# Kernel optimization log

Measured on AMD Instinct MI355X. Metric: run time of the kernel, lower is better.

The kernel has to match this reference:

```python
import jax, jax.numpy as jnp
import numpy as np

B, IN, OUT = 1024, 512, 64000
EPS = 1e-12  # matches torch F.normalize eps


def setup_inputs() -> dict:
    key = jax.random.key(0)
    k1, k2, k3 = jax.random.split(key, 3)
    x = jax.random.normal(k1, (B, IN), dtype=jnp.float32)
    label = jax.random.randint(k2, (B,), 0, OUT)
    # xavier_uniform_ for weight [OUT, IN]: limit = sqrt(6 / (fan_in + fan_out))
    limit = float(np.sqrt(6.0 / (IN + OUT)))
    weight = jax.random.uniform(k3, (OUT, IN), dtype=jnp.float32, minval=-limit, maxval=limit)
    s = 50               # python scalar; set via _calculate_para but UNUSED in normfree output
    m = jnp.full((1,), 0.5, dtype=jnp.float32)  # margin
    return {"x": x, "label": label, "weight": weight, "s": s, "m": m}


def reference(x, label, weight, s, m):
    m = m.reshape(())
    cos_m, sin_m = jnp.cos(m), jnp.sin(m)
    # norm of raw input (the 'normfree' scale replacing s)
    norm = jnp.linalg.norm(x, axis=1, keepdims=True)            # [B, 1]
    xn = x / jnp.maximum(norm, EPS)                             # F.normalize(input)
    wn = weight / jnp.maximum(
        jnp.linalg.norm(weight, axis=1, keepdims=True), EPS)    # F.normalize(weight)
    cosine = xn @ wn.T                                          # [B, OUT]
    sine = jnp.sqrt(jnp.clip(1.0 - cosine * cosine, 0.0, None))
    phi = cosine * cos_m - sine * sin_m                         # cos(theta + m)
    # per-sample loop in torch == one-hot substitution only where cosine > 0
    onehot = jax.nn.one_hot(label, OUT, dtype=bool)             # [B, OUT]
    mod_cosine = jnp.where(onehot & (cosine > 0), phi, cosine)
    return norm * mod_cosine, wn
```

## Files before the change

kernel.cpp:

```cpp
#include <hip/hip_runtime.h>
#include <cstdint>

#define EPSN 1e-12f
static constexpr int B_ROWS = 1024;
static constexpr int IN_DIM = 512;
static constexpr int OUT_DIM = 64000;

typedef __attribute__((ext_vector_type(8))) short bf16x8;
typedef __attribute__((ext_vector_type(4))) float f32x4;

__device__ __forceinline__ unsigned short f2bf(float f) {
  uint32_t u = __builtin_bit_cast(uint32_t, f);
  u += 0x7fffu + ((u >> 16) & 1u);
  return (unsigned short)(u >> 16);
}

__device__ __forceinline__ float wave_sum(float v) {
#pragma unroll
  for (int off = 32; off; off >>= 1) v += __shfl_xor(v, off);
  return v;
}

__device__ __forceinline__ void async16(const void* g, void* l) {
  __builtin_amdgcn_global_load_lds((const __attribute__((address_space(1))) uint32_t*)g,
                                   (__attribute__((address_space(3))) uint32_t*)l, 16, 0, 0);
}

__global__ void wnorm_kernel(const float* __restrict__ Wg, float* __restrict__ wnOut,
                             unsigned short* __restrict__ wbf, int useBf) {
  int lane = threadIdx.x & 63;
  int row = blockIdx.x * 4 + (threadIdx.x >> 6);
  const float* src = Wg + (size_t)row * IN_DIM + lane * 8;
  float4 a = *(const float4*)src;
  float4 b = *(const float4*)(src + 4);
  float ss = a.x * a.x;
  ss = fmaf(a.y, a.y, ss); ss = fmaf(a.z, a.z, ss); ss = fmaf(a.w, a.w, ss);
  ss = fmaf(b.x, b.x, ss); ss = fmaf(b.y, b.y, ss); ss = fmaf(b.z, b.z, ss);
  ss = fmaf(b.w, b.w, ss);
  ss = wave_sum(ss);
  float inv = 1.0f / fmaxf(sqrtf(ss), EPSN);
  float4 wa, wb;
  wa.x = a.x * inv; wa.y = a.y * inv; wa.z = a.z * inv; wa.w = a.w * inv;
  wb.x = b.x * inv; wb.y = b.y * inv; wb.z = b.z * inv; wb.w = b.w * inv;
  float* dst = wnOut + (size_t)row * IN_DIM + lane * 8;
  *(float4*)dst = wa;
  *(float4*)(dst + 4) = wb;
  if (useBf) {
    uint4 u;
    u.x = (uint32_t)f2bf(wa.x) | ((uint32_t)f2bf(wa.y) << 16);
    u.y = (uint32_t)f2bf(wa.z) | ((uint32_t)f2bf(wa.w) << 16);
    u.z = (uint32_t)f2bf(wb.x) | ((uint32_t)f2bf(wb.y) << 16);
    u.w = (uint32_t)f2bf(wb.z) | ((uint32_t)f2bf(wb.w) << 16);
    *(uint4*)(wbf + (size_t)row * IN_DIM + lane * 8) = u;
  }
}

__global__ void prep_kernel(const float* __restrict__ X, const int* __restrict__ label,
                            const float* __restrict__ wn, float* __restrict__ norms,
                            float* __restrict__ fixdot, unsigned short* __restrict__ xbf) {
  int lane = threadIdx.x & 63;
  int row = blockIdx.x * 4 + (threadIdx.x >> 6);
  const float* src = X + (size_t)row * IN_DIM + lane * 8;
  float4 a = *(const float4*)src;
  float4 b = *(const float4*)(src + 4);
  uint4 u;
  u.x = (uint32_t)f2bf(a.x) | ((uint32_t)f2bf(a.y) << 16);
  u.y = (uint32_t)f2bf(a.z) | ((uint32_t)f2bf(a.w) << 16);
  u.z = (uint32_t)f2bf(b.x) | ((uint32_t)f2bf(b.y) << 16);
  u.w = (uint32_t)f2bf(b.z) | ((uint32_t)f2bf(b.w) << 16);
  *(uint4*)(xbf + (size_t)row * IN_DIM + lane * 8) = u;
  float ss = a.x * a.x;
  ss = fmaf(a.y, a.y, ss); ss = fmaf(a.z, a.z, ss); ss = fmaf(a.w, a.w, ss);
  ss = fmaf(b.x, b.x, ss); ss = fmaf(b.y, b.y, ss); ss = fmaf(b.z, b.z, ss);
  ss = fmaf(b.w, b.w, ss);
  ss = wave_sum(ss);
  int lab = label[row];
  const float* wsrc = wn + (size_t)lab * IN_DIM + lane * 8;
  float4 wa = *(const float4*)wsrc, wb = *(const float4*)(wsrc + 4);
  float d = a.x * wa.x;
  d = fmaf(a.y, wa.y, d); d = fmaf(a.z, wa.z, d); d = fmaf(a.w, wa.w, d);
  d = fmaf(b.x, wb.x, d); d = fmaf(b.y, wb.y, d); d = fmaf(b.z, wb.z, d);
  d = fmaf(b.w, wb.w, d);
  d = wave_sum(d);
  if (lane == 0) { norms[row] = sqrtf(ss); fixdot[row] = d; }
}

template <bool BF16B>
__global__ __launch_bounds__(512, 2) void gemm8_kernel(
    const unsigned short* __restrict__ Abf, const unsigned short* __restrict__ Bbf,
    const float* __restrict__ Bf32, const float* __restrict__ norms,
    const float* __restrict__ fixdot, const int* __restrict__ label,
    const float* __restrict__ mArr, float* __restrict__ out0) {
  __shared__ char smem[131072];

  const int t = threadIdx.x;
  int flat = blockIdx.x;
  int xcd = flat & 7;
  int wk = (flat >> 3) + xcd * 125;
  int mT = wk & 3, nT = wk >> 2;
  int rowA0 = mT * 256, rowB0 = nT * 256;

  int lane = t & 63;
  int wid = t >> 6;
  int wm = wid >> 2, wn2 = wid & 3;
  int rl = lane & 15, sl = lane >> 4;

  int r0 = t >> 2, q0 = (t & 3) ^ ((r0 >> 1) & 3);
  int r1 = (t + 512) >> 2, q1 = ((t + 512) & 3) ^ ((r1 >> 1) & 3);
  const unsigned short* aP0 = Abf + (size_t)(rowA0 + r0) * IN_DIM + q0 * 8;
  const unsigned short* aP1 = Abf + (size_t)(rowA0 + r1) * IN_DIM + q1 * 8;
  const unsigned short* bP0 = Bbf + (size_t)(rowB0 + r0) * IN_DIM + q0 * 8;
  const unsigned short* bP1 = Bbf + (size_t)(rowB0 + r1) * IN_DIM + q1 * 8;
  const float* bF0 = Bf32 + (size_t)(rowB0 + r0) * IN_DIM + q0 * 8;
  const float* bF1 = Bf32 + (size_t)(rowB0 + r1) * IN_DIM + q1 * 8;

  auto issueSub = [&](int sig) {
    int kt = sig >> 1, s = sig & 1, buf = kt & 1;
    char* aD = smem + buf * 65536 + s * 16384;
    char* bD = aD + 32768;
    int kcol = kt * 64 + s * 32;
    async16(aP0 + kcol, aD + t * 16);
    async16(aP1 + kcol, aD + (t + 512) * 16);
    if constexpr (BF16B) {
      async16(bP0 + kcol, bD + t * 16);
      async16(bP1 + kcol, bD + (t + 512) * 16);
    } else {
      float4 f0 = *(const float4*)(bF0 + kcol);
      float4 f1 = *(const float4*)(bF0 + kcol + 4);
      uint4 u;
      u.x = (uint32_t)f2bf(f0.x) | ((uint32_t)f2bf(f0.y) << 16);
      u.y = (uint32_t)f2bf(f0.z) | ((uint32_t)f2bf(f0.w) << 16);
      u.z = (uint32_t)f2bf(f1.x) | ((uint32_t)f2bf(f1.y) << 16);
      u.w = (uint32_t)f2bf(f1.z) | ((uint32_t)f2bf(f1.w) << 16);
      *(uint4*)(bD + t * 16) = u;
      f0 = *(const float4*)(bF1 + kcol);
      f1 = *(const float4*)(bF1 + kcol + 4);
      u.x = (uint32_t)f2bf(f0.x) | ((uint32_t)f2bf(f0.y) << 16);
      u.y = (uint32_t)f2bf(f0.z) | ((uint32_t)f2bf(f0.w) << 16);
      u.z = (uint32_t)f2bf(f1.x) | ((uint32_t)f2bf(f1.y) << 16);
      u.w = (uint32_t)f2bf(f1.z) | ((uint32_t)f2bf(f1.w) << 16);
      *(uint4*)(bD + (t + 512) * 16) = u;
    }
  };

  issueSub(0); issueSub(1); issueSub(2);

  f32x4 acc[8][4];
#pragma unroll
  for (int m = 0; m < 8; ++m)
#pragma unroll
    for (int n = 0; n < 4; ++n) acc[m][n] = (f32x4){0.f, 0.f, 0.f, 0.f};

#pragma unroll 1
  for (int sigma = 0; sigma < 16; ++sigma) {
    int kt = sigma >> 1, s = sigma & 1, buf = kt & 1;
    if constexpr (BF16B) {
      int remain = 15 - sigma;
      __builtin_amdgcn_sched_barrier(0);
      if (remain >= 2)      asm volatile("s_waitcnt vmcnt(8)" ::: "memory");
      else if (remain == 1) asm volatile("s_waitcnt vmcnt(4)" ::: "memory");
      else                  asm volatile("s_waitcnt vmcnt(0)" ::: "memory");
      __builtin_amdgcn_s_barrier();
      __builtin_amdgcn_sched_barrier(0);
    } else {
      __syncthreads();
    }
    const char* aB = smem + buf * 65536 + s * 16384;
    const char* bB = aB + 32768;
    bf16x8 av[8], bv[4];
#pragma unroll
    for (int m = 0; m < 8; ++m) {
      int r = wm * 128 + m * 16 + rl;
      av[m] = *(const bf16x8*)(aB + r * 64 + ((sl ^ ((r >> 1) & 3)) * 16));
    }
#pragma unroll
    for (int n = 0; n < 4; ++n) {
      int r = wn2 * 64 + n * 16 + rl;
      bv[n] = *(const bf16x8*)(bB + r * 64 + ((sl ^ ((r >> 1) & 3)) * 16));
    }
    if (sigma + 3 <= 15) issueSub(sigma + 3);
    __builtin_amdgcn_s_setprio(1);
#pragma unroll
    for (int n = 0; n < 4; ++n)
#pragma unroll
      for (int m = 0; m < 8; ++m)
        acc[m][n] = __builtin_amdgcn_mfma_f32_16x16x32_bf16(av[m], bv[n], acc[m][n], 0, 0, 0);
    __builtin_amdgcn_s_setprio(0);
    if constexpr (BF16B) {
      __builtin_amdgcn_s_barrier();
      __builtin_amdgcn_sched_barrier(0);
    } else {
      __syncthreads();
    }
  }

  float mm = mArr[0];
  float cm = cosf(mm), sm = sinf(mm);
  int rowb = rowA0 + wm * 128, colb = rowB0 + wn2 * 64;
#pragma unroll
  for (int m = 0; m < 8; ++m) {
#pragma unroll
    for (int q = 0; q < 4; ++q) {
      int R = rowb + m * 16 + sl * 4 + q;
      int lab = label[R];
      float nv = norms[R], fv = fixdot[R];
      float* orow = out0 + (size_t)R * OUT_DIM;
#pragma unroll
      for (int n = 0; n < 4; ++n) {
        int Cc = colb + n * 16 + rl;
        float val = acc[m][n][q];
        if (Cc == lab) {
          float c = fv / fmaxf(nv, EPSN);
          val = (c > 0.f) ? nv * (c * cm - sqrtf(fmaxf(1.f - c * c, 0.f)) * sm) : fv;
        }
        orow[Cc] = val;
      }
    }
  }
}

extern "C" void kernel_launch(void* const* d_in, const int* in_sizes, int n_in,
                              void* d_out, int out_size, void* d_ws, size_t ws_size,
                              hipStream_t stream) {
  const float* x = (const float*)d_in[0];
  const int* label = (const int*)d_in[1];
  const float* weight = (const float*)d_in[2];
  const float* mArr = (const float*)d_in[4];

  float* out0 = (float*)d_out;
  float* wnOut = out0 + (size_t)B_ROWS * OUT_DIM;

  char* ws = (char*)d_ws;
  float* norms = (float*)ws;
  float* fixdot = (float*)(ws + 4096);
  unsigned short* xbf = (unsigned short*)(ws + 8192);
  unsigned short* wbf = (unsigned short*)(ws + 8192 + 2ull * B_ROWS * IN_DIM);
  size_t need = 8192 + 2ull * B_ROWS * IN_DIM + 2ull * OUT_DIM * IN_DIM;
  bool useBf = ws_size >= need;

  wnorm_kernel<<<OUT_DIM / 4, 256, 0, stream>>>(weight, wnOut, wbf, useBf ? 1 : 0);
  prep_kernel<<<B_ROWS / 4, 256, 0, stream>>>(x, label, wnOut, norms, fixdot, xbf);
  if (useBf)
    gemm8_kernel<true><<<1000, 512, 0, stream>>>(xbf, wbf, wnOut, norms, fixdot,
                                                 label, mArr, out0);
  else
    gemm8_kernel<false><<<1000, 512, 0, stream>>>(xbf, wbf, wnOut, norms, fixdot,
                                                  label, mArr, out0);
}
```

Before: 199.0 us.

## Fuse weight normalization into GEMM, staging normalized bf16 B tiles in-kernel

Drops the separate weight-normalization kernel and the bf16 weight copy in workspace. Each GEMM block now computes inverse row norms for its 256 weight rows, writes one quarter of the normalized fp32 rows to the wn output, and converts fp32 weight to scaled bf16 while staging B into LDS with a 4-deep ring buffer. The prep kernel computes the label-row norm itself so it no longer depends on wn. This removes a full read-write pass over the 131MB weight plus the bf16 write and re-read. In exchange each weight tile is read in fp32 by all four M-tile blocks, with synchronous register-path B loads in the main loop and an extra norm pass at the start of every block.

Measured after the change: 284.5 us. +43.0%, slower.

```diff
diff --git a/kernel.cpp b/kernel.cpp
--- a/kernel.cpp
+++ b/kernel.cpp
@@ -26,37 +26,8 @@
                                    (__attribute__((address_space(3))) uint32_t*)l, 16, 0, 0);
 }
 
-__global__ void wnorm_kernel(const float* __restrict__ Wg, float* __restrict__ wnOut,
-                             unsigned short* __restrict__ wbf, int useBf) {
-  int lane = threadIdx.x & 63;
-  int row = blockIdx.x * 4 + (threadIdx.x >> 6);
-  const float* src = Wg + (size_t)row * IN_DIM + lane * 8;
-  float4 a = *(const float4*)src;
-  float4 b = *(const float4*)(src + 4);
-  float ss = a.x * a.x;
-  ss = fmaf(a.y, a.y, ss); ss = fmaf(a.z, a.z, ss); ss = fmaf(a.w, a.w, ss);
-  ss = fmaf(b.x, b.x, ss); ss = fmaf(b.y, b.y, ss); ss = fmaf(b.z, b.z, ss);
-  ss = fmaf(b.w, b.w, ss);
-  ss = wave_sum(ss);
-  float inv = 1.0f / fmaxf(sqrtf(ss), EPSN);
-  float4 wa, wb;
-  wa.x = a.x * inv; wa.y = a.y * inv; wa.z = a.z * inv; wa.w = a.w * inv;
-  wb.x = b.x * inv; wb.y = b.y * inv; wb.z = b.z * inv; wb.w = b.w * inv;
-  float* dst = wnOut + (size_t)row * IN_DIM + lane * 8;
-  *(float4*)dst = wa;
-  *(float4*)(dst + 4) = wb;
-  if (useBf) {
-    uint4 u;
-    u.x = (uint32_t)f2bf(wa.x) | ((uint32_t)f2bf(wa.y) << 16);
-    u.y = (uint32_t)f2bf(wa.z) | ((uint32_t)f2bf(wa.w) << 16);
-    u.z = (uint32_t)f2bf(wb.x) | ((uint32_t)f2bf(wb.y) << 16);
-    u.w = (uint32_t)f2bf(wb.z) | ((uint32_t)f2bf(wb.w) << 16);
-    *(uint4*)(wbf + (size_t)row * IN_DIM + lane * 8) = u;
-  }
-}
-
 __global__ void prep_kernel(const float* __restrict__ X, const int* __restrict__ label,
-                            const float* __restrict__ wn, float* __restrict__ norms,
+                            const float* __restrict__ Wg, float* __restrict__ norms,
                             float* __restrict__ fixdot, unsigned short* __restrict__ xbf) {
   int lane = threadIdx.x & 63;
   int row = blockIdx.x * 4 + (threadIdx.x >> 6);
@@ -69,29 +40,37 @@
   u.z = (uint32_t)f2bf(b.x) | ((uint32_t)f2bf(b.y) << 16);
   u.w = (uint32_t)f2bf(b.z) | ((uint32_t)f2bf(b.w) << 16);
   *(uint4*)(xbf + (size_t)row * IN_DIM + lane * 8) = u;
-  float ss = a.x * a.x;
-  ss = fmaf(a.y, a.y, ss); ss = fmaf(a.z, a.z, ss); ss = fmaf(a.w, a.w, ss);
-  ss = fmaf(b.x, b.x, ss); ss = fmaf(b.y, b.y, ss); ss = fmaf(b.z, b.z, ss);
-  ss = fmaf(b.w, b.w, ss);
-  ss = wave_sum(ss);
+  float ssx = a.x * a.x;
+  ssx = fmaf(a.y, a.y, ssx); ssx = fmaf(a.z, a.z, ssx); ssx = fmaf(a.w, a.w, ssx);
+  ssx = fmaf(b.x, b.x, ssx); ssx = fmaf(b.y, b.y, ssx); ssx = fmaf(b.z, b.z, ssx);
+  ssx = fmaf(b.w, b.w, ssx);
   int lab = label[row];
-  const float* wsrc = wn + (size_t)lab * IN_DIM + lane * 8;
+  const float* wsrc = Wg + (size_t)lab * IN_DIM + lane * 8;
   float4 wa = *(const float4*)wsrc, wb = *(const float4*)(wsrc + 4);
   float d = a.x * wa.x;
   d = fmaf(a.y, wa.y, d); d = fmaf(a.z, wa.z, d); d = fmaf(a.w, wa.w, d);
   d = fmaf(b.x, wb.x, d); d = fmaf(b.y, wb.y, d); d = fmaf(b.z, wb.z, d);
   d = fmaf(b.w, wb.w, d);
+  float ssw = wa.x * wa.x;
+  ssw = fmaf(wa.y, wa.y, ssw); ssw = fmaf(wa.z, wa.z, ssw); ssw = fmaf(wa.w, wa.w, ssw);
+  ssw = fmaf(wb.x, wb.x, ssw); ssw = fmaf(wb.y, wb.y, ssw); ssw = fmaf(wb.z, wb.z, ssw);
+  ssw = fmaf(wb.w, wb.w, ssw);
+  ssx = wave_sum(ssx);
   d = wave_sum(d);
-  if (lane == 0) { norms[row] = sqrtf(ss); fixdot[row] = d; }
-}
-
-template <bool BF16B>
-__global__ __launch_bounds__(512, 2) void gemm8_kernel(
-    const unsigned short* __restrict__ Abf, const unsigned short* __restrict__ Bbf,
-    const float* __restrict__ Bf32, const float* __restrict__ norms,
-    const float* __restrict__ fixdot, const int* __restrict__ label,
-    const float* __restrict__ mArr, float* __restrict__ out0) {
-  __shared__ char smem[131072];
+  ssw = wave_sum(ssw);
+  if (lane == 0) {
+    norms[row] = sqrtf(ssx);
+    fixdot[row] = d / fmaxf(sqrtf(ssw), EPSN);
+  }
+}
+
+__global__ __launch_bounds__(512, 2) void fused_kernel(
+    const float* __restrict__ Wg, const unsigned short* __restrict__ Abf,
+    const float* __restrict__ norms, const float* __restrict__ fixdot,
+    const int* __restrict__ label, const float* __restrict__ mArr,
+    float* __restrict__ out0, float* __restrict__ wnOut) {
+  __shared__ char smem[132096];
+  float* invnL = (float*)(smem + 131072);
 
   const int t = threadIdx.x;
   int flat = blockIdx.x;
@@ -105,45 +84,72 @@
   int wm = wid >> 2, wn2 = wid & 3;
   int rl = lane & 15, sl = lane >> 4;
 
-  int r0 = t >> 2, q0 = (t & 3) ^ ((r0 >> 1) & 3);
-  int r1 = (t + 512) >> 2, q1 = ((t + 512) & 3) ^ ((r1 >> 1) & 3);
-  const unsigned short* aP0 = Abf + (size_t)(rowA0 + r0) * IN_DIM + q0 * 8;
-  const unsigned short* aP1 = Abf + (size_t)(rowA0 + r1) * IN_DIM + q1 * 8;
-  const unsigned short* bP0 = Bbf + (size_t)(rowB0 + r0) * IN_DIM + q0 * 8;
-  const unsigned short* bP1 = Bbf + (size_t)(rowB0 + r1) * IN_DIM + q1 * 8;
-  const float* bF0 = Bf32 + (size_t)(rowB0 + r0) * IN_DIM + q0 * 8;
-  const float* bF1 = Bf32 + (size_t)(rowB0 + r1) * IN_DIM + q1 * 8;
-
-  auto issueSub = [&](int sig) {
-    int kt = sig >> 1, s = sig & 1, buf = kt & 1;
-    char* aD = smem + buf * 65536 + s * 16384;
-    char* bD = aD + 32768;
-    int kcol = kt * 64 + s * 32;
+#pragma unroll 1
+  for (int rr = 0; rr < 32; ++rr) {
+    int r = wid * 32 + rr;
+    const float* src = Wg + (size_t)(rowB0 + r) * IN_DIM + lane * 8;
+    float4 a = *(const float4*)src;
+    float4 b = *(const float4*)(src + 4);
+    float ss = a.x * a.x;
+    ss = fmaf(a.y, a.y, ss); ss = fmaf(a.z, a.z, ss); ss = fmaf(a.w, a.w, ss);
+    ss = fmaf(b.x, b.x, ss); ss = fmaf(b.y, b.y, ss); ss = fmaf(b.z, b.z, ss);
+    ss = fmaf(b.w, b.w, ss);
+    ss = wave_sum(ss);
+    float inv = 1.0f / fmaxf(sqrtf(ss), EPSN);
+    if (lane == 0) invnL[r] = inv;
+    if ((r >> 6) == mT) {
+      float* dst = wnOut + (size_t)(rowB0 + r) * IN_DIM + lane * 8;
+      float4 wa, wb;
+      wa.x = a.x * inv; wa.y = a.y * inv; wa.z = a.z * inv; wa.w = a.w * inv;
+      wb.x = b.x * inv; wb.y = b.y * inv; wb.z = b.z * inv; wb.w = b.w * inv;
+      *(float4*)dst = wa;
+      *(float4*)(dst + 4) = wb;
+    }
+  }
+  __syncthreads();
+
+  int r0 = t >> 2, q0 = t & 3;
+  int r1 = (t + 512) >> 2, q1 = (t + 512) & 3;
+  float inv0 = invnL[r0], inv1 = invnL[r1];
+  const float* bSrc0 = Wg + (size_t)(rowB0 + r0) * IN_DIM + q0 * 8;
+  const float* bSrc1 = Wg + (size_t)(rowB0 + r1) * IN_DIM + q1 * 8;
+  int bOff0 = r0 * 64 + ((q0 ^ ((r0 >> 1) & 3)) * 16);
+  int bOff1 = r1 * 64 + ((q1 ^ ((r1 >> 1) & 3)) * 16);
+
+  int ra0 = t >> 2, qa0 = (t & 3) ^ ((ra0 >> 1) & 3);
+  int ra1 = (t + 512) >> 2, qa1 = ((t + 512) & 3) ^ ((ra1 >> 1) & 3);
+  const unsigned short* aP0 = Abf + (size_t)(rowA0 + ra0) * IN_DIM + qa0 * 8;
+  const unsigned short* aP1 = Abf + (size_t)(rowA0 + ra1) * IN_DIM + qa1 * 8;
+
+  auto issueA = [&](int sig) {
+    char* aD = smem + (sig & 3) * 16384;
+    int kcol = sig * 32;
     async16(aP0 + kcol, aD + t * 16);
     async16(aP1 + kcol, aD + (t + 512) * 16);
-    if constexpr (BF16B) {
-      async16(bP0 + kcol, bD + t * 16);
-      async16(bP1 + kcol, bD + (t + 512) * 16);
-    } else {
-      float4 f0 = *(const float4*)(bF0 + kcol);
-      float4 f1 = *(const float4*)(bF0 + kcol + 4);
-      uint4 u;
-      u.x = (uint32_t)f2bf(f0.x) | ((uint32_t)f2bf(f0.y) << 16);
-      u.y = (uint32_t)f2bf(f0.z) | ((uint32_t)f2bf(f0.w) << 16);
-      u.z = (uint32_t)f2bf(f1.x) | ((uint32_t)f2bf(f1.y) << 16);
-      u.w = (uint32_t)f2bf(f1.z) | ((uint32_t)f2bf(f1.w) << 16);
-      *(uint4*)(bD + t * 16) = u;
-      f0 = *(const float4*)(bF1 + kcol);
-      f1 = *(const float4*)(bF1 + kcol + 4);
-      u.x = (uint32_t)f2bf(f0.x) | ((uint32_t)f2bf(f0.y) << 16);
-      u.y = (uint32_t)f2bf(f0.z) | ((uint32_t)f2bf(f0.w) << 16);
-      u.z = (uint32_t)f2bf(f1.x) | ((uint32_t)f2bf(f1.y) << 16);
-      u.w = (uint32_t)f2bf(f1.z) | ((uint32_t)f2bf(f1.w) << 16);
-      *(uint4*)(bD + (t + 512) * 16) = u;
-    }
   };
-
-  issueSub(0); issueSub(1); issueSub(2);
+  auto stageB = [&](int sig) {
+    char* bD = smem + 65536 + (sig & 3) * 16384;
+    int kcol = sig * 32;
+    float4 f0 = *(const float4*)(bSrc0 + kcol);
+    float4 f1 = *(const float4*)(bSrc0 + kcol + 4);
+    uint4 u;
+    u.x = (uint32_t)f2bf(f0.x * inv0) | ((uint32_t)f2bf(f0.y * inv0) << 16);
+    u.y = (uint32_t)f2bf(f0.z * inv0) | ((uint32_t)f2bf(f0.w * inv0) << 16);
+    u.z = (uint32_t)f2bf(f1.x * inv0) | ((uint32_t)f2bf(f1.y * inv0) << 16);
+    u.w = (uint32_t)f2bf(f1.z * inv0) | ((uint32_t)f2bf(f1.w * inv0) << 16);
+    *(uint4*)(bD + bOff0) = u;
+    f0 = *(const float4*)(bSrc1 + kcol);
+    f1 = *(const float4*)(bSrc1 + kcol + 4);
+    u.x = (uint32_t)f2bf(f0.x * inv1) | ((uint32_t)f2bf(f0.y * inv1) << 16);
+    u.y = (uint32_t)f2bf(f0.z * inv1) | ((uint32_t)f2bf(f0.w * inv1) << 16);
+    u.z = (uint32_t)f2bf(f1.x * inv1) | ((uint32_t)f2bf(f1.y * inv1) << 16);
+    u.w = (uint32_t)f2bf(f1.z * inv1) | ((uint32_t)f2bf(f1.w * inv1) << 16);
+    *(uint4*)(bD + bOff1) = u;
+  };
+
+  issueA(0); issueA(1); issueA(2);
+  stageB(0);
+  asm volatile("s_waitcnt lgkmcnt(0)" ::: "memory");
 
   f32x4 acc[8][4];
 #pragma unroll
@@ -153,20 +159,15 @@
 
 #pragma unroll 1
   for (int sigma = 0; sigma < 16; ++sigma) {
-    int kt = sigma >> 1, s = sigma & 1, buf = kt & 1;
-    if constexpr (BF16B) {
-      int remain = 15 - sigma;
-      __builtin_amdgcn_sched_barrier(0);
-      if (remain >= 2)      asm volatile("s_waitcnt vmcnt(8)" ::: "memory");
-      else if (remain == 1) asm volatile("s_waitcnt vmcnt(4)" ::: "memory");
-      else                  asm volatile("s_waitcnt vmcnt(0)" ::: "memory");
-      __builtin_amdgcn_s_barrier();
-      __builtin_amdgcn_sched_barrier(0);
-    } else {
-      __syncthreads();
-    }
-    const char* aB = smem + buf * 65536 + s * 16384;
-    const char* bB = aB + 32768;
+    __builtin_amdgcn_sched_barrier(0);
+    if (sigma <= 13)      asm volatile("s_waitcnt vmcnt(4)" ::: "memory");
+    else if (sigma == 14) asm volatile("s_waitcnt vmcnt(2)" ::: "memory");
+    else                  asm volatile("s_waitcnt vmcnt(0)" ::: "memory");
+    __builtin_amdgcn_s_barrier();
+    __builtin_amdgcn_sched_barrier(0);
+
+    const char* aB = smem + (sigma & 3) * 16384;
+    const char* bB = smem + 65536 + (sigma & 3) * 16384;
     bf16x8 av[8], bv[4];
 #pragma unroll
     for (int m = 0; m < 8; ++m) {
@@ -178,7 +179,8 @@
       int r = wn2 * 64 + n * 16 + rl;
       bv[n] = *(const bf16x8*)(bB + r * 64 + ((sl ^ ((r >> 1) & 3)) * 16));
     }
-    if (sigma + 3 <= 15) issueSub(sigma + 3);
+    if (sigma + 3 <= 15) issueA(sigma + 3);
+    if (sigma + 1 <= 15) stageB(sigma + 1);
     __builtin_amdgcn_s_setprio(1);
 #pragma unroll
     for (int n = 0; n < 4; ++n)
@@ -186,12 +188,9 @@
       for (int m = 0; m < 8; ++m)
         acc[m][n] = __builtin_amdgcn_mfma_f32_16x16x32_bf16(av[m], bv[n], acc[m][n], 0, 0, 0);
     __builtin_amdgcn_s_setprio(0);
-    if constexpr (BF16B) {
-      __builtin_amdgcn_s_barrier();
-      __builtin_amdgcn_sched_barrier(0);
-    } else {
-      __syncthreads();
-    }
+    asm volatile("s_waitcnt lgkmcnt(0)" ::: "memory");
+    __builtin_amdgcn_s_barrier();
+    __builtin_amdgcn_sched_barrier(0);
   }
 
   float mm = mArr[0];
@@ -234,16 +233,8 @@
   float* norms = (float*)ws;
   float* fixdot = (float*)(ws + 4096);
   unsigned short* xbf = (unsigned short*)(ws + 8192);
-  unsigned short* wbf = (unsigned short*)(ws + 8192 + 2ull * B_ROWS * IN_DIM);
-  size_t need = 8192 + 2ull * B_ROWS * IN_DIM + 2ull * OUT_DIM * IN_DIM;
-  bool useBf = ws_size >= need;
-
-  wnorm_kernel<<<OUT_DIM / 4, 256, 0, stream>>>(weight, wnOut, wbf, useBf ? 1 : 0);
-  prep_kernel<<<B_ROWS / 4, 256, 0, stream>>>(x, label, wnOut, norms, fixdot, xbf);
-  if (useBf)
-    gemm8_kernel<true><<<1000, 512, 0, stream>>>(xbf, wbf, wnOut, norms, fixdot,
-                                                 label, mArr, out0);
-  else
-    gemm8_kernel<false><<<1000, 512, 0, stream>>>(xbf, wbf, wnOut, norms, fixdot,
-                                                  label, mArr, out0);
-}
+
+  prep_kernel<<<B_ROWS / 4, 256, 0, stream>>>(x, label, weight, norms, fixdot, xbf);
+  fused_kernel<<<1000, 512, 0, stream>>>(weight, xbf, norms, fixdot, label, mArr,
+                                         out0, wnOut);
+}
```
